# Kernel optimization log

Hardware: AMD Instinct MI355X
Metric: run time of the kernel (lower is better)

The kernel has to match this reference:

```python
import jax, jax.numpy as jnp
import numpy as np

B = 8
S_MAX = 1024
H = 12
HD = 64
D = H * HD
DFF = 4 * D
NEG = -1.0e9  # matches Triton kernel's -1000000000.0 mask value


def _layernorm(x, g, b, eps=1e-6):
    mu = jnp.mean(x, axis=-1, keepdims=True)
    var = jnp.mean((x - mu) ** 2, axis=-1, keepdims=True)
    return (x - mu) * jax.lax.rsqrt(var + eps) * g + b


def setup_inputs() -> dict:
    key = jax.random.key(0)
    ks = jax.random.split(key, 12)
    lengths = np.array([1024, 896, 768, 640, 896, 1024, 512, 384], dtype=np.int32)
    assert lengths.max() <= S_MAX and len(lengths) == B
    total = int(lengths.sum())  # 6144
    cu = jnp.asarray(np.concatenate([[0], np.cumsum(lengths)]), dtype=jnp.int32)
    s = 0.02
    return {
        "x": jax.random.normal(ks[0], (total, D), jnp.float32),
        "cu_seqlens": cu,
        "g1": jnp.ones((D,), jnp.float32),
        "beta1": jnp.zeros((D,), jnp.float32),
        "Wqkv": jax.random.normal(ks[1], (D, 3 * D), jnp.float32) * s,
        "bqkv": jnp.zeros((3 * D,), jnp.float32),
        "Wo": jax.random.normal(ks[2], (D, D), jnp.float32) * s,
        "bo": jnp.zeros((D,), jnp.float32),
        "g2": jnp.ones((D,), jnp.float32),
        "beta2": jnp.zeros((D,), jnp.float32),
        "W1": jax.random.normal(ks[3], (D, DFF), jnp.float32) * s,
        "b_fc1": jnp.zeros((DFF,), jnp.float32),
        "W2": jax.random.normal(ks[4], (DFF, D), jnp.float32) * s,
        "b_fc2": jnp.zeros((D,), jnp.float32),
    }


def _ragged_attention(q, k, v, cu_seqlens):
    # q,k,v: [Total, H, HD] packed ragged sequences; cu_seqlens: [B+1] int32
    total = q.shape[0]
    lens = cu_seqlens[1:] - cu_seqlens[:-1]                      # [B]
    s = jnp.arange(S_MAX)
    pad_idx = cu_seqlens[:-1, None] + jnp.minimum(s[None, :], lens[:, None] - 1)  # [B,S]
    valid = s[None, :] < lens[:, None]                           # [B,S]
    qp = q[pad_idx]                                              # [B,S,H,HD]
    kp = k[pad_idx]
    vp = v[pad_idx]
    scale = 1.0 / jnp.sqrt(jnp.float32(HD))
    scores = jnp.einsum("bqhd,bkhd->bhqk", qp, kp) * scale      # [B,H,S,S]
    scores = jnp.where(valid[:, None, None, :], scores, NEG)     # mask invalid keys
    p = jax.nn.softmax(scores, axis=-1)
    op = jnp.einsum("bhqk,bkhd->bqhd", p, vp)                   # [B,S,H,HD]
    # repack to [Total, H, HD]
    tok = jnp.arange(total)
    seg = jnp.searchsorted(cu_seqlens, tok, side="right") - 1    # sequence id per token
    pos = tok - cu_seqlens[seg]
    return op[seg, pos]


def _forward(x, cu_seqlens, g1, beta1, Wqkv, bqkv, Wo, bo, g2, beta2, W1, b_fc1, W2, b_fc2):
    total = x.shape[0]
    qkv = (_layernorm(x, g1, beta1) @ Wqkv + bqkv).reshape(total, 3, H, HD)
    q, k, v = qkv[:, 0], qkv[:, 1], qkv[:, 2]
    attn = _ragged_attention(q, k, v, cu_seqlens).reshape(total, D)
    x = x + (attn @ Wo + bo)                                     # proj_drop/ls1/drop_path identity (eval)
    h = _layernorm(x, g2, beta2)
    m = jax.nn.gelu(h @ W1 + b_fc1, approximate=False)
    return x + (m @ W2 + b_fc2)


def reference(x, cu_seqlens, g1, beta1, Wqkv, bqkv, Wo, bo, g2, beta2, W1, b_fc1, W2, b_fc2):
    return _forward(x, cu_seqlens, g1, beta1, Wqkv, bqkv, Wo, bo, g2, beta2, W1, b_fc1, W2, b_fc2)
```

## Files before the change

kernel.cpp:

```cpp
#include <hip/hip_runtime.h>
#include <hip/hip_bf16.h>
#include <stdint.h>
#include <string.h>

#define D_MODEL 768
#define H_HEADS 12
#define HD_ 64
#define N_QKV 2304

typedef __bf16 bf16x8 __attribute__((ext_vector_type(8)));
typedef float f32x4 __attribute__((ext_vector_type(4)));

__device__ __forceinline__ void gload16(const void* gsrc, void* ldst) {
  __builtin_amdgcn_global_load_lds(
      (__attribute__((address_space(1))) void*)gsrc,
      (__attribute__((address_space(3))) void*)ldst, 16, 0, 0);
}

__device__ __forceinline__ unsigned short f2bfbits(float f) {
  union { float f; unsigned u; } x; x.f = f;
  unsigned r = x.u + 0x7fffu + ((x.u >> 16) & 1u);
  return (unsigned short)(r >> 16);
}

__device__ __forceinline__ unsigned pk2(float a, float b) {
  union { float f; unsigned u; } x, y; x.f = a; y.f = b;
  return ((x.u + 0x8000u) >> 16) | ((y.u + 0x8000u) & 0xffff0000u);
}

__device__ __forceinline__ f32x4 vmax4(f32x4 a, f32x4 b) {
  f32x4 r;
  r[0] = fmaxf(a[0], b[0]); r[1] = fmaxf(a[1], b[1]);
  r[2] = fmaxf(a[2], b[2]); r[3] = fmaxf(a[3], b[3]);
  return r;
}

__global__ void transpose_w(const float* __restrict__ in, unsigned short* __restrict__ out,
                            int R, int C) {
  __shared__ float tile[32][33];
  int c0 = blockIdx.x * 32, r0 = blockIdx.y * 32;
  int tx = threadIdx.x, ty = threadIdx.y;
#pragma unroll
  for (int i = 0; i < 32; i += 8)
    tile[ty + i][tx] = in[(size_t)(r0 + ty + i) * C + c0 + tx];
  __syncthreads();
#pragma unroll
  for (int i = 0; i < 32; i += 8)
    out[(size_t)(c0 + ty + i) * R + r0 + tx] = f2bfbits(tile[tx][ty + i]);
}

__global__ void transpose_v(const unsigned short* __restrict__ qkv,
                            unsigned short* __restrict__ vT, int M) {
  __shared__ unsigned short tile[32][33];
  int t0 = blockIdx.x * 32, c0 = blockIdx.y * 32;
  int tx = threadIdx.x, ty = threadIdx.y;
#pragma unroll
  for (int i = 0; i < 32; i += 8)
    tile[ty + i][tx] = qkv[(size_t)(t0 + ty + i) * N_QKV + 1536 + c0 + tx];
  __syncthreads();
  int t = t0 + tx;
  int c = t & 63;
  int kp = ((c >> 5) << 5) | (((c >> 2) & 3) << 3) | (((c >> 4) & 1) << 2) | (c & 3);
  size_t col = (size_t)(t & ~63) + kp;
#pragma unroll
  for (int i = 0; i < 32; i += 8)
    vT[(size_t)(c0 + ty + i) * M + col] = tile[tx][ty + i];
}

__global__ void ln_bf16(const float* __restrict__ x, const float* __restrict__ g,
                        const float* __restrict__ be, unsigned short* __restrict__ out) {
  int row = blockIdx.x;
  const float* xr = x + (size_t)row * D_MODEL;
  int t = threadIdx.x;
  float v0 = xr[t], v1 = xr[t + 256], v2 = xr[t + 512];
  float s = v0 + v1 + v2;
  float s2 = v0 * v0 + v1 * v1 + v2 * v2;
#pragma unroll
  for (int off = 32; off > 0; off >>= 1) {
    s += __shfl_down(s, off, 64);
    s2 += __shfl_down(s2, off, 64);
  }
  __shared__ float red[8];
  int w = t >> 6, lane = t & 63;
  if (lane == 0) { red[w] = s; red[w + 4] = s2; }
  __syncthreads();
  if (t == 0) {
    float a = red[0] + red[1] + red[2] + red[3];
    float b = red[4] + red[5] + red[6] + red[7];
    red[0] = a * (1.0f / 768.0f);
    red[4] = b * (1.0f / 768.0f);
  }
  __syncthreads();
  float mu = red[0];
  float var = red[4] - mu * mu;
  float rs = rsqrtf(var + 1e-6f);
  unsigned short* orow = out + (size_t)row * D_MODEL;
  orow[t]       = f2bfbits((v0 - mu) * rs * g[t]       + be[t]);
  orow[t + 256] = f2bfbits((v1 - mu) * rs * g[t + 256] + be[t + 256]);
  orow[t + 512] = f2bfbits((v2 - mu) * rs * g[t + 512] + be[t + 512]);
}

template <int EPI>
__global__ void gemm_bt(const unsigned short* __restrict__ A,
                        const unsigned short* __restrict__ Bt,
                        const float* __restrict__ bias,
                        const float* __restrict__ res,
                        void* __restrict__ outv,
                        int M, int N, int K) {
  __shared__ unsigned short lA[128 * 32];
  __shared__ unsigned short lB[128 * 32];
  int tid = threadIdx.x;
  int w = tid >> 6, lane = tid & 63;
  int m0 = blockIdx.y * 128, n0 = blockIdx.x * 128;
  int wm = (w >> 1) * 64, wn = (w & 1) * 64;
  f32x4 acc[4][4];
#pragma unroll
  for (int i = 0; i < 4; i++)
#pragma unroll
    for (int j = 0; j < 4; j++) acc[i][j] = (f32x4){0.f, 0.f, 0.f, 0.f};

  int srow = tid >> 2, scol = (tid & 3) * 8;
  const unsigned short* gA0 = A + (size_t)(m0 + srow) * K + scol;
  const unsigned short* gB0 = Bt + (size_t)(n0 + srow) * K + scol;
  char* lA0 = (char*)lA + tid * 16;
  char* lB0 = (char*)lB + tid * 16;
  int fm = lane & 15, fk = (lane >> 4) * 8;

  for (int k0 = 0; k0 < K; k0 += 32) {
    __syncthreads();
    gload16(gA0 + k0, lA0);
    gload16(gA0 + (size_t)64 * K + k0, lA0 + 4096);
    gload16(gB0 + k0, lB0);
    gload16(gB0 + (size_t)64 * K + k0, lB0 + 4096);
    __syncthreads();
    bf16x8 af[4], bfr[4];
#pragma unroll
    for (int i = 0; i < 4; i++)
      af[i] = *(const bf16x8*)&lA[(wm + i * 16 + fm) * 32 + fk];
#pragma unroll
    for (int j = 0; j < 4; j++)
      bfr[j] = *(const bf16x8*)&lB[(wn + j * 16 + fm) * 32 + fk];
#pragma unroll
    for (int i = 0; i < 4; i++)
#pragma unroll
      for (int j = 0; j < 4; j++)
        acc[i][j] = __builtin_amdgcn_mfma_f32_16x16x32_bf16(af[i], bfr[j], acc[i][j], 0, 0, 0);
  }

  int er = (lane >> 4) * 4, ec = lane & 15;
#pragma unroll
  for (int i = 0; i < 4; i++) {
#pragma unroll
    for (int j = 0; j < 4; j++) {
      int n = n0 + wn + j * 16 + ec;
      float bv = bias[n];
#pragma unroll
      for (int r = 0; r < 4; r++) {
        int m = m0 + wm + i * 16 + er + r;
        float v = acc[i][j][r] + bv;
        if (EPI == 1) {
          v += res[(size_t)m * N + n];
          ((float*)outv)[(size_t)m * N + n] = v;
        } else {
          if (EPI == 2) v = 0.5f * v * (1.0f + erff(v * 0.70710678118f));
          ((unsigned short*)outv)[(size_t)m * N + n] = f2bfbits(v);
        }
      }
    }
  }
}

__global__ void attn_flash2(const unsigned short* __restrict__ qkv,
                            const unsigned short* __restrict__ vT,
                            const int* __restrict__ cu,
                            unsigned short* __restrict__ out, int M) {
  int qc = blockIdx.x & 7;
  int h = (blockIdx.x >> 3) % H_HEADS;
  int b = blockIdx.x / (8 * H_HEADS);
  int tok0 = cu[b];
  int len = cu[b + 1] - tok0;
  if (qc * 128 >= len) return;

  __shared__ unsigned short lK[64 * 64];
  __shared__ unsigned short lVT[64 * 64];

  int tid = threadIdx.x, w = tid >> 6, lane = tid & 63;
  int fm = lane & 15, fg = lane >> 4;
  int xm = fm & 7;
  int qbase = qc * 128 + w * 32;

  bf16x8 qf[2][2];
#pragma unroll
  for (int qs = 0; qs < 2; qs++)
#pragma unroll
    for (int kh = 0; kh < 2; kh++)
      qf[qs][kh] = *(const bf16x8*)(qkv + (size_t)(tok0 + qbase + qs * 16 + fm) * N_QKV +
                                    h * 64 + kh * 32 + fg * 8);

  f32x4 Oacc[2][4];
#pragma unroll
  for (int qs = 0; qs < 2; qs++)
#pragma unroll
    for (int dt = 0; dt < 4; dt++) Oacc[qs][dt] = (f32x4){0.f, 0.f, 0.f, 0.f};
  float mrow[2] = {-1e30f, -1e30f}, lrow[2] = {0.f, 0.f};
  const float C2 = 0.18033688011112042f;

  int sr = tid >> 3, sp = tid & 7, sl = sp ^ (sr & 7);
  const unsigned short* kg0 = qkv + D_MODEL + h * 64 + sl * 8;
  const unsigned short* vg0 = vT + (size_t)(h * 64 + sr) * M + tok0 + sl * 8;
  char* lK0 = (char*)lK + tid * 16;
  char* lV0 = (char*)lVT + tid * 16;

  for (int kt = 0; kt < len; kt += 64) {
    __syncthreads();
    gload16(kg0 + (size_t)(tok0 + kt + sr) * N_QKV, lK0);
    gload16(kg0 + (size_t)(tok0 + kt + sr + 32) * N_QKV, lK0 + 4096);
    gload16(vg0 + kt, lV0);
    gload16(vg0 + (size_t)32 * M + kt, lV0 + 4096);
    __syncthreads();

    f32x4 s[2][4];
#pragma unroll
    for (int qs = 0; qs < 2; qs++)
#pragma unroll
      for (int t = 0; t < 4; t++) s[qs][t] = (f32x4){0.f, 0.f, 0.f, 0.f};
#pragma unroll
    for (int t = 0; t < 4; t++) {
      bf16x8 kf0 = *(const bf16x8*)&lK[(t * 16 + fm) * 64 + ((fg ^ xm) * 8)];
      bf16x8 kf1 = *(const bf16x8*)&lK[(t * 16 + fm) * 64 + (((4 + fg) ^ xm) * 8)];
#pragma unroll
      for (int qs = 0; qs < 2; qs++) {
        s[qs][t] = __builtin_amdgcn_mfma_f32_16x16x32_bf16(kf0, qf[qs][0], s[qs][t], 0, 0, 0);
        s[qs][t] = __builtin_amdgcn_mfma_f32_16x16x32_bf16(kf1, qf[qs][1], s[qs][t], 0, 0, 0);
      }
    }

    unsigned pkv[2][4][2];
#pragma unroll
    for (int qs = 0; qs < 2; qs++) {
      f32x4 m4 = vmax4(vmax4(s[qs][0], s[qs][1]), vmax4(s[qs][2], s[qs][3]));
      float mx = fmaxf(fmaxf(m4[0], m4[1]), fmaxf(m4[2], m4[3]));
      mx = fmaxf(mx, __shfl_xor(mx, 16, 64));
      mx = fmaxf(mx, __shfl_xor(mx, 32, 64));
      float mnew = fmaxf(mrow[qs], mx);
      float al = exp2f((mrow[qs] - mnew) * C2);
      mrow[qs] = mnew;
      float nm = mnew * C2;
      float ssum = 0.f;
#pragma unroll
      for (int t = 0; t < 4; t++) {
#pragma unroll
        for (int r = 0; r < 4; r++) {
          float p = exp2f(s[qs][t][r] * C2 - nm);
          s[qs][t][r] = p;
          ssum += p;
        }
        pkv[qs][t][0] = pk2(s[qs][t][0], s[qs][t][1]);
        pkv[qs][t][1] = pk2(s[qs][t][2], s[qs][t][3]);
      }
      ssum += __shfl_xor(ssum, 16, 64);
      ssum += __shfl_xor(ssum, 32, 64);
      lrow[qs] = lrow[qs] * al + ssum;
      float ar[4];
#pragma unroll
      for (int r = 0; r < 4; r++) ar[r] = __shfl(al, fg * 4 + r, 64);
#pragma unroll
      for (int dt = 0; dt < 4; dt++) {
        Oacc[qs][dt][0] *= ar[0]; Oacc[qs][dt][1] *= ar[1];
        Oacc[qs][dt][2] *= ar[2]; Oacc[qs][dt][3] *= ar[3];
      }
    }

    union { bf16x8 v; unsigned u[4]; } af[2][2];
#pragma unroll
    for (int qs = 0; qs < 2; qs++) {
      af[qs][0].u[0] = pkv[qs][0][0]; af[qs][0].u[1] = pkv[qs][0][1];
      af[qs][0].u[2] = pkv[qs][1][0]; af[qs][0].u[3] = pkv[qs][1][1];
      af[qs][1].u[0] = pkv[qs][2][0]; af[qs][1].u[1] = pkv[qs][2][1];
      af[qs][1].u[2] = pkv[qs][3][0]; af[qs][1].u[3] = pkv[qs][3][1];
    }
#pragma unroll
    for (int dt = 0; dt < 4; dt++) {
      bf16x8 vf0 = *(const bf16x8*)&lVT[(dt * 16 + fm) * 64 + ((fg ^ xm) * 8)];
      bf16x8 vf1 = *(const bf16x8*)&lVT[(dt * 16 + fm) * 64 + (((4 + fg) ^ xm) * 8)];
#pragma unroll
      for (int qs = 0; qs < 2; qs++) {
        Oacc[qs][dt] = __builtin_amdgcn_mfma_f32_16x16x32_bf16(af[qs][0].v, vf0, Oacc[qs][dt], 0, 0, 0);
        Oacc[qs][dt] = __builtin_amdgcn_mfma_f32_16x16x32_bf16(af[qs][1].v, vf1, Oacc[qs][dt], 0, 0, 0);
      }
    }
  }

#pragma unroll
  for (int qs = 0; qs < 2; qs++) {
    float inv = 1.0f / lrow[qs];
    float ir[4];
#pragma unroll
    for (int r = 0; r < 4; r++) ir[r] = __shfl(inv, fg * 4 + r, 64);
#pragma unroll
    for (int dt = 0; dt < 4; dt++)
#pragma unroll
      for (int r = 0; r < 4; r++)
        out[(size_t)(tok0 + qbase + qs * 16 + fg * 4 + r) * D_MODEL + h * 64 + dt * 16 + fm] =
            f2bfbits(Oacc[qs][dt][r] * ir[r]);
  }
}

extern "C" void kernel_launch(void* const* d_in, const int* in_sizes, int n_in,
                              void* d_out, int out_size, void* d_ws, size_t ws_size,
                              hipStream_t stream) {
  const float* x    = (const float*)d_in[0];
  const int* cu     = (const int*)d_in[1];
  const float* g1   = (const float*)d_in[2];
  const float* be1  = (const float*)d_in[3];
  const float* Wqkv = (const float*)d_in[4];
  const float* bqkv = (const float*)d_in[5];
  const float* Wo   = (const float*)d_in[6];
  const float* bo   = (const float*)d_in[7];
  const float* g2   = (const float*)d_in[8];
  const float* be2  = (const float*)d_in[9];
  const float* W1   = (const float*)d_in[10];
  const float* bfc1 = (const float*)d_in[11];
  const float* W2   = (const float*)d_in[12];
  const float* bfc2 = (const float*)d_in[13];
  float* out = (float*)d_out;
  int M = in_sizes[0] / D_MODEL;

  unsigned short* WqkvT = (unsigned short*)d_ws;
  unsigned short* WoT   = WqkvT + 2304 * 768;
  unsigned short* W1T   = WoT + 768 * 768;
  unsigned short* W2T   = W1T + 3072 * 768;
  unsigned short* bufA  = W2T + 768 * 3072;
  float* x1             = (float*)(bufA + (size_t)M * D_MODEL);
  unsigned short* qkvb  = (unsigned short*)(x1 + (size_t)M * D_MODEL);
  unsigned short* vT = (unsigned short*)x1;

  dim3 b32(32, 8);
  transpose_w<<<dim3(2304 / 32, 768 / 32), b32, 0, stream>>>(Wqkv, WqkvT, 768, 2304);
  transpose_w<<<dim3(768 / 32, 768 / 32), b32, 0, stream>>>(Wo, WoT, 768, 768);
  transpose_w<<<dim3(3072 / 32, 768 / 32), b32, 0, stream>>>(W1, W1T, 768, 3072);
  transpose_w<<<dim3(768 / 32, 3072 / 32), b32, 0, stream>>>(W2, W2T, 3072, 768);

  ln_bf16<<<M, 256, 0, stream>>>(x, g1, be1, bufA);
  gemm_bt<0><<<dim3(2304 / 128, M / 128), 256, 0, stream>>>(bufA, WqkvT, bqkv, nullptr, qkvb, M, 2304, 768);
  transpose_v<<<dim3(M / 32, 768 / 32), b32, 0, stream>>>(qkvb, vT, M);
  attn_flash2<<<8 * H_HEADS * 8, 256, 0, stream>>>(qkvb, vT, cu, bufA, M);
  gemm_bt<1><<<dim3(768 / 128, M / 128), 256, 0, stream>>>(bufA, WoT, bo, x, x1, M, 768, 768);
  ln_bf16<<<M, 256, 0, stream>>>(x1, g2, be2, bufA);
  gemm_bt<2><<<dim3(3072 / 128, M / 128), 256, 0, stream>>>(bufA, W1T, bfc1, nullptr, qkvb, M, 3072, 768);
  gemm_bt<1><<<dim3(768 / 128, M / 128), 256, 0, stream>>>(qkvb, W2T, bfc2, x1, out, M, 768, 3072);
}
```

Measured before the change: 380.6 us.

## Double-buffer GEMM LDS tiles and use 256-row tiles for wide GEMMs

The GEMM kernel now keeps two LDS buffers. It issues the global-to-LDS loads for the next K slice before computing on the current one, which cuts the barriers per iteration from two to one and overlaps memory traffic with MFMA work. The kernel is also templated on the M tile. The QKV and FC1 GEMMs use 256-row tiles with 512 threads, which doubles the reuse of each B tile. The cost is twice the LDS per block, plus fewer and larger blocks for those GEMMs, so fewer blocks are in flight.

New measurement: 381.0 us. Within noise of the previous version (+0.1%).

```diff
diff --git a/kernel.cpp b/kernel.cpp
--- a/kernel.cpp
+++ b/kernel.cpp
@@ -100,18 +100,19 @@
   orow[t + 512] = f2bfbits((v2 - mu) * rs * g[t + 512] + be[t + 512]);
 }
 
-template <int EPI>
-__global__ void gemm_bt(const unsigned short* __restrict__ A,
-                        const unsigned short* __restrict__ Bt,
-                        const float* __restrict__ bias,
-                        const float* __restrict__ res,
-                        void* __restrict__ outv,
-                        int M, int N, int K) {
-  __shared__ unsigned short lA[128 * 32];
-  __shared__ unsigned short lB[128 * 32];
+template <int EPI, int TM>
+__global__ void __launch_bounds__(TM * 2, 4)
+gemm_bt(const unsigned short* __restrict__ A,
+        const unsigned short* __restrict__ Bt,
+        const float* __restrict__ bias,
+        const float* __restrict__ res,
+        void* __restrict__ outv,
+        int M, int N, int K) {
+  __shared__ unsigned short lA[2][TM * 32];
+  __shared__ unsigned short lB[2][128 * 32];
   int tid = threadIdx.x;
   int w = tid >> 6, lane = tid & 63;
-  int m0 = blockIdx.y * 128, n0 = blockIdx.x * 128;
+  int m0 = blockIdx.y * TM, n0 = blockIdx.x * 128;
   int wm = (w >> 1) * 64, wn = (w & 1) * 64;
   f32x4 acc[4][4];
 #pragma unroll
@@ -122,29 +123,35 @@
   int srow = tid >> 2, scol = (tid & 3) * 8;
   const unsigned short* gA0 = A + (size_t)(m0 + srow) * K + scol;
   const unsigned short* gB0 = Bt + (size_t)(n0 + srow) * K + scol;
-  char* lA0 = (char*)lA + tid * 16;
-  char* lB0 = (char*)lB + tid * 16;
   int fm = lane & 15, fk = (lane >> 4) * 8;
 
+  auto stage = [&](int buf, int k0) {
+    char* a0 = (char*)&lA[buf][0] + tid * 16;
+    char* b0 = (char*)&lB[buf][0] + tid * 16;
+    gload16(gA0 + k0, a0);
+    gload16(gA0 + (size_t)(TM / 2) * K + k0, a0 + (TM / 2) * 64);
+    gload16(gB0 + k0, b0);
+    if (TM == 128) gload16(gB0 + (size_t)64 * K + k0, b0 + 4096);
+  };
+
+  stage(0, 0);
+  int nb = 0;
   for (int k0 = 0; k0 < K; k0 += 32) {
     __syncthreads();
-    gload16(gA0 + k0, lA0);
-    gload16(gA0 + (size_t)64 * K + k0, lA0 + 4096);
-    gload16(gB0 + k0, lB0);
-    gload16(gB0 + (size_t)64 * K + k0, lB0 + 4096);
-    __syncthreads();
+    if (k0 + 32 < K) stage(nb ^ 1, k0 + 32);
     bf16x8 af[4], bfr[4];
 #pragma unroll
     for (int i = 0; i < 4; i++)
-      af[i] = *(const bf16x8*)&lA[(wm + i * 16 + fm) * 32 + fk];
+      af[i] = *(const bf16x8*)&lA[nb][(wm + i * 16 + fm) * 32 + fk];
 #pragma unroll
     for (int j = 0; j < 4; j++)
-      bfr[j] = *(const bf16x8*)&lB[(wn + j * 16 + fm) * 32 + fk];
+      bfr[j] = *(const bf16x8*)&lB[nb][(wn + j * 16 + fm) * 32 + fk];
 #pragma unroll
     for (int i = 0; i < 4; i++)
 #pragma unroll
       for (int j = 0; j < 4; j++)
         acc[i][j] = __builtin_amdgcn_mfma_f32_16x16x32_bf16(af[i], bfr[j], acc[i][j], 0, 0, 0);
+    nb ^= 1;
   }
 
   int er = (lane >> 4) * 4, ec = lane & 15;
@@ -342,11 +349,11 @@
   transpose_w<<<dim3(768 / 32, 3072 / 32), b32, 0, stream>>>(W2, W2T, 3072, 768);
 
   ln_bf16<<<M, 256, 0, stream>>>(x, g1, be1, bufA);
-  gemm_bt<0><<<dim3(2304 / 128, M / 128), 256, 0, stream>>>(bufA, WqkvT, bqkv, nullptr, qkvb, M, 2304, 768);
+  gemm_bt<0, 256><<<dim3(2304 / 128, M / 256), 512, 0, stream>>>(bufA, WqkvT, bqkv, nullptr, qkvb, M, 2304, 768);
   transpose_v<<<dim3(M / 32, 768 / 32), b32, 0, stream>>>(qkvb, vT, M);
   attn_flash2<<<8 * H_HEADS * 8, 256, 0, stream>>>(qkvb, vT, cu, bufA, M);
-  gemm_bt<1><<<dim3(768 / 128, M / 128), 256, 0, stream>>>(bufA, WoT, bo, x, x1, M, 768, 768);
+  gemm_bt<1, 128><<<dim3(768 / 128, M / 128), 256, 0, stream>>>(bufA, WoT, bo, x, x1, M, 768, 768);
   ln_bf16<<<M, 256, 0, stream>>>(x1, g2, be2, bufA);
-  gemm_bt<2><<<dim3(3072 / 128, M / 128), 256, 0, stream>>>(bufA, W1T, bfc1, nullptr, qkvb, M, 3072, 768);
-  gemm_bt<1><<<dim3(768 / 128, M / 128), 256, 0, stream>>>(qkvb, W2T, bfc2, x1, out, M, 768, 3072);
-}
+  gemm_bt<2, 256><<<dim3(3072 / 128, M / 256), 512, 0, stream>>>(bufA, W1T, bfc1, nullptr, qkvb, M, 3072, 768);
+  gemm_bt<1, 128><<<dim3(768 / 128, M / 128), 256, 0, stream>>>(qkvb, W2T, bfc2, x1, out, M, 768, 3072);
+}
```

## Give each wave private double-buffered LDS tiles and drop block barriers in GEMM

Applied to the files above, without the earlier changes.

The GEMM kernel now has each wave load its own 64x32 A and B slices into a per-wave, double-buffered LDS region. Waves synchronise with s_waitcnt instead of __syncthreads, so loading the next K step overlaps the MFMA work on the current one. The cost is loss of A/B tile sharing across waves: each wave fetches its own copies, which doubles global traffic per block and quadruples LDS use to 64 KB. Launch bounds request two blocks per CU.

Result: slower. 435.9 us (+14.5%).

```diff
diff --git a/kernel.cpp b/kernel.cpp
--- a/kernel.cpp
+++ b/kernel.cpp
@@ -101,45 +101,59 @@
 }
 
 template <int EPI>
-__global__ void gemm_bt(const unsigned short* __restrict__ A,
-                        const unsigned short* __restrict__ Bt,
-                        const float* __restrict__ bias,
-                        const float* __restrict__ res,
-                        void* __restrict__ outv,
-                        int M, int N, int K) {
-  __shared__ unsigned short lA[128 * 32];
-  __shared__ unsigned short lB[128 * 32];
+__global__ void __launch_bounds__(256, 2)
+gemm_wp(const unsigned short* __restrict__ A,
+        const unsigned short* __restrict__ Bt,
+        const float* __restrict__ bias,
+        const float* __restrict__ res,
+        void* __restrict__ outv,
+        int M, int N, int K) {
+  __shared__ unsigned short lds[4][2][2][64 * 32];
   int tid = threadIdx.x;
   int w = tid >> 6, lane = tid & 63;
-  int m0 = blockIdx.y * 128, n0 = blockIdx.x * 128;
-  int wm = (w >> 1) * 64, wn = (w & 1) * 64;
+  int m0 = blockIdx.y * 128 + (w >> 1) * 64;
+  int n0 = blockIdx.x * 128 + (w & 1) * 64;
   f32x4 acc[4][4];
 #pragma unroll
   for (int i = 0; i < 4; i++)
 #pragma unroll
     for (int j = 0; j < 4; j++) acc[i][j] = (f32x4){0.f, 0.f, 0.f, 0.f};
 
-  int srow = tid >> 2, scol = (tid & 3) * 8;
-  const unsigned short* gA0 = A + (size_t)(m0 + srow) * K + scol;
-  const unsigned short* gB0 = Bt + (size_t)(n0 + srow) * K + scol;
-  char* lA0 = (char*)lA + tid * 16;
-  char* lB0 = (char*)lB + tid * 16;
+  const unsigned short* gA = A + (size_t)(m0 + (lane >> 2)) * K + (lane & 3) * 8;
+  const unsigned short* gB = Bt + (size_t)(n0 + (lane >> 2)) * K + (lane & 3) * 8;
   int fm = lane & 15, fk = (lane >> 4) * 8;
 
-  for (int k0 = 0; k0 < K; k0 += 32) {
-    __syncthreads();
-    gload16(gA0 + k0, lA0);
-    gload16(gA0 + (size_t)64 * K + k0, lA0 + 4096);
-    gload16(gB0 + k0, lB0);
-    gload16(gB0 + (size_t)64 * K + k0, lB0 + 4096);
-    __syncthreads();
+  auto stage = [&](int d, int k0) {
+    char* aB = (char*)&lds[w][d][0][0] + lane * 16;
+    char* bB = (char*)&lds[w][d][1][0] + lane * 16;
+#pragma unroll
+    for (int j = 0; j < 4; j++)
+      gload16(gA + (size_t)(j * 16) * K + k0, aB + j * 1024);
+#pragma unroll
+    for (int j = 0; j < 4; j++)
+      gload16(gB + (size_t)(j * 16) * K + k0, bB + j * 1024);
+  };
+
+  int nk = K >> 5;
+  stage(0, 0);
+  for (int k = 0; k < nk; k++) {
+    int cur = k & 1;
+    if (k + 1 < nk) {
+      asm volatile("s_waitcnt lgkmcnt(0)" ::: "memory");
+      stage(cur ^ 1, (k + 1) * 32);
+      asm volatile("s_waitcnt vmcnt(8)" ::: "memory");
+    } else {
+      asm volatile("s_waitcnt vmcnt(0)" ::: "memory");
+    }
+    const unsigned short* la = &lds[w][cur][0][0];
+    const unsigned short* lb = &lds[w][cur][1][0];
     bf16x8 af[4], bfr[4];
 #pragma unroll
     for (int i = 0; i < 4; i++)
-      af[i] = *(const bf16x8*)&lA[(wm + i * 16 + fm) * 32 + fk];
+      af[i] = *(const bf16x8*)&la[(i * 16 + fm) * 32 + fk];
 #pragma unroll
     for (int j = 0; j < 4; j++)
-      bfr[j] = *(const bf16x8*)&lB[(wn + j * 16 + fm) * 32 + fk];
+      bfr[j] = *(const bf16x8*)&lb[(j * 16 + fm) * 32 + fk];
 #pragma unroll
     for (int i = 0; i < 4; i++)
 #pragma unroll
@@ -152,11 +166,11 @@
   for (int i = 0; i < 4; i++) {
 #pragma unroll
     for (int j = 0; j < 4; j++) {
-      int n = n0 + wn + j * 16 + ec;
+      int n = n0 + j * 16 + ec;
       float bv = bias[n];
 #pragma unroll
       for (int r = 0; r < 4; r++) {
-        int m = m0 + wm + i * 16 + er + r;
+        int m = m0 + i * 16 + er + r;
         float v = acc[i][j][r] + bv;
         if (EPI == 1) {
           v += res[(size_t)m * N + n];
@@ -342,11 +356,11 @@
   transpose_w<<<dim3(768 / 32, 3072 / 32), b32, 0, stream>>>(W2, W2T, 3072, 768);
 
   ln_bf16<<<M, 256, 0, stream>>>(x, g1, be1, bufA);
-  gemm_bt<0><<<dim3(2304 / 128, M / 128), 256, 0, stream>>>(bufA, WqkvT, bqkv, nullptr, qkvb, M, 2304, 768);
+  gemm_wp<0><<<dim3(2304 / 128, M / 128), 256, 0, stream>>>(bufA, WqkvT, bqkv, nullptr, qkvb, M, 2304, 768);
   transpose_v<<<dim3(M / 32, 768 / 32), b32, 0, stream>>>(qkvb, vT, M);
   attn_flash2<<<8 * H_HEADS * 8, 256, 0, stream>>>(qkvb, vT, cu, bufA, M);
-  gemm_bt<1><<<dim3(768 / 128, M / 128), 256, 0, stream>>>(bufA, WoT, bo, x, x1, M, 768, 768);
+  gemm_wp<1><<<dim3(768 / 128, M / 128), 256, 0, stream>>>(bufA, WoT, bo, x, x1, M, 768, 768);
   ln_bf16<<<M, 256, 0, stream>>>(x1, g2, be2, bufA);
-  gemm_bt<2><<<dim3(3072 / 128, M / 128), 256, 0, stream>>>(bufA, W1T, bfc1, nullptr, qkvb, M, 3072, 768);
-  gemm_bt<1><<<dim3(768 / 128, M / 128), 256, 0, stream>>>(qkvb, W2T, bfc2, x1, out, M, 768, 3072);
-}
+  gemm_wp<2><<<dim3(3072 / 128, M / 128), 256, 0, stream>>>(bufA, W1T, bfc1, nullptr, qkvb, M, 3072, 768);
+  gemm_wp<1><<<dim3(768 / 128, M / 128), 256, 0, stream>>>(qkvb, W2T, bfc2, x1, out, M, 768, 3072);
+}
```

## Double-buffer GEMM LDS tiles via register prefetch with XOR swizzle

Applied to the files above, without the earlier changes.

The GEMM main loop replaces direct global-to-LDS loads and two barriers per iteration with register-staged prefetch. The next K-slice is loaded into registers while the current one is consumed, and there is one barrier per step into double-buffered LDS. LDS rows use an XOR swizzle to reduce bank conflicts on the bf16x8 fragment reads, and launch bounds target 3 blocks per CU. This adds register pressure and relies on an inline waitcnt/barrier sequence for correct ordering.

After: 366.3 us. 1.04x faster.

```diff
diff --git a/kernel.cpp b/kernel.cpp
--- a/kernel.cpp
+++ b/kernel.cpp
@@ -101,14 +101,15 @@
 }
 
 template <int EPI>
-__global__ void gemm_bt(const unsigned short* __restrict__ A,
-                        const unsigned short* __restrict__ Bt,
-                        const float* __restrict__ bias,
-                        const float* __restrict__ res,
-                        void* __restrict__ outv,
-                        int M, int N, int K) {
-  __shared__ unsigned short lA[128 * 32];
-  __shared__ unsigned short lB[128 * 32];
+__global__ void __launch_bounds__(256, 3)
+gemm_rs(const unsigned short* __restrict__ A,
+        const unsigned short* __restrict__ Bt,
+        const float* __restrict__ bias,
+        const float* __restrict__ res,
+        void* __restrict__ outv,
+        int M, int N, int K) {
+  __shared__ unsigned short lA[2][128 * 32];
+  __shared__ unsigned short lB[2][128 * 32];
   int tid = threadIdx.x;
   int w = tid >> 6, lane = tid & 63;
   int m0 = blockIdx.y * 128, n0 = blockIdx.x * 128;
@@ -119,27 +120,43 @@
 #pragma unroll
     for (int j = 0; j < 4; j++) acc[i][j] = (f32x4){0.f, 0.f, 0.f, 0.f};
 
-  int srow = tid >> 2, scol = (tid & 3) * 8;
-  const unsigned short* gA0 = A + (size_t)(m0 + srow) * K + scol;
-  const unsigned short* gB0 = Bt + (size_t)(n0 + srow) * K + scol;
-  char* lA0 = (char*)lA + tid * 16;
-  char* lB0 = (char*)lB + tid * 16;
-  int fm = lane & 15, fk = (lane >> 4) * 8;
-
-  for (int k0 = 0; k0 < K; k0 += 32) {
-    __syncthreads();
-    gload16(gA0 + k0, lA0);
-    gload16(gA0 + (size_t)64 * K + k0, lA0 + 4096);
-    gload16(gB0 + k0, lB0);
-    gload16(gB0 + (size_t)64 * K + k0, lB0 + 4096);
-    __syncthreads();
+  int sr = tid >> 2, sc = tid & 3;
+  const unsigned short* gA = A + (size_t)(m0 + sr) * K + sc * 8;
+  const unsigned short* gB = Bt + (size_t)(n0 + sr) * K + sc * 8;
+  int wOff = sr * 64 + ((((sr >> 1) & 3) ^ sc) * 16);
+  int fm = lane & 15, fg = lane >> 4;
+
+  uint4 ra0, ra1, rb0, rb1;
+  auto gload = [&](int k0) {
+    ra0 = *(const uint4*)(gA + k0);
+    ra1 = *(const uint4*)(gA + (size_t)64 * K + k0);
+    rb0 = *(const uint4*)(gB + k0);
+    rb1 = *(const uint4*)(gB + (size_t)64 * K + k0);
+  };
+
+  int nk = K >> 5;
+  gload(0);
+  for (int k = 0; k < nk; k++) {
+    int cur = k & 1;
+    char* la = (char*)&lA[cur][0];
+    char* lb = (char*)&lB[cur][0];
+    *(uint4*)(la + wOff) = ra0;
+    *(uint4*)(la + wOff + 4096) = ra1;
+    *(uint4*)(lb + wOff) = rb0;
+    *(uint4*)(lb + wOff + 4096) = rb1;
+    if (k + 1 < nk) gload((k + 1) * 32);
+    asm volatile("s_waitcnt lgkmcnt(0)\ns_barrier" ::: "memory");
     bf16x8 af[4], bfr[4];
 #pragma unroll
-    for (int i = 0; i < 4; i++)
-      af[i] = *(const bf16x8*)&lA[(wm + i * 16 + fm) * 32 + fk];
-#pragma unroll
-    for (int j = 0; j < 4; j++)
-      bfr[j] = *(const bf16x8*)&lB[(wn + j * 16 + fm) * 32 + fk];
+    for (int i = 0; i < 4; i++) {
+      int rr = wm + i * 16 + fm;
+      af[i] = *(const bf16x8*)(la + rr * 64 + ((((rr >> 1) & 3) ^ fg) * 16));
+    }
+#pragma unroll
+    for (int j = 0; j < 4; j++) {
+      int rr = wn + j * 16 + fm;
+      bfr[j] = *(const bf16x8*)(lb + rr * 64 + ((((rr >> 1) & 3) ^ fg) * 16));
+    }
 #pragma unroll
     for (int i = 0; i < 4; i++)
 #pragma unroll
@@ -342,11 +359,11 @@
   transpose_w<<<dim3(768 / 32, 3072 / 32), b32, 0, stream>>>(W2, W2T, 3072, 768);
 
   ln_bf16<<<M, 256, 0, stream>>>(x, g1, be1, bufA);
-  gemm_bt<0><<<dim3(2304 / 128, M / 128), 256, 0, stream>>>(bufA, WqkvT, bqkv, nullptr, qkvb, M, 2304, 768);
+  gemm_rs<0><<<dim3(2304 / 128, M / 128), 256, 0, stream>>>(bufA, WqkvT, bqkv, nullptr, qkvb, M, 2304, 768);
   transpose_v<<<dim3(M / 32, 768 / 32), b32, 0, stream>>>(qkvb, vT, M);
   attn_flash2<<<8 * H_HEADS * 8, 256, 0, stream>>>(qkvb, vT, cu, bufA, M);
-  gemm_bt<1><<<dim3(768 / 128, M / 128), 256, 0, stream>>>(bufA, WoT, bo, x, x1, M, 768, 768);
+  gemm_rs<1><<<dim3(768 / 128, M / 128), 256, 0, stream>>>(bufA, WoT, bo, x, x1, M, 768, 768);
   ln_bf16<<<M, 256, 0, stream>>>(x1, g2, be2, bufA);
-  gemm_bt<2><<<dim3(3072 / 128, M / 128), 256, 0, stream>>>(bufA, W1T, bfc1, nullptr, qkvb, M, 3072, 768);
-  gemm_bt<1><<<dim3(768 / 128, M / 128), 256, 0, stream>>>(qkvb, W2T, bfc2, x1, out, M, 768, 3072);
-}
+  gemm_rs<2><<<dim3(3072 / 128, M / 128), 256, 0, stream>>>(bufA, W1T, bfc1, nullptr, qkvb, M, 3072, 768);
+  gemm_rs<1><<<dim3(768 / 128, M / 128), 256, 0, stream>>>(qkvb, W2T, bfc2, x1, out, M, 768, 3072);
+}
```
